# Performance work log

Hardware: AMD Instinct MI355X
Metric: run time of the kernel (lower is better)

The kernel has to match this reference:

```python
import jax, jax.numpy as jnp
import numpy as np

N = 50_000
E = 1_600_000
C_IN, C_HID, C_OUT, M = 128, 128, 2, 4


def gcn_norm(edge_index, num_nodes):
    # GCNConv default: add self-loops, symmetric normalization D^-1/2 (A+I) D^-1/2
    src, dst = edge_index[0], edge_index[1]
    loop = jnp.arange(num_nodes, dtype=edge_index.dtype)
    src = jnp.concatenate([src, loop])
    dst = jnp.concatenate([dst, loop])
    deg = jax.ops.segment_sum(jnp.ones_like(dst, dtype=jnp.float32), dst,
                              num_segments=num_nodes)
    dinv = jnp.where(deg > 0, jax.lax.rsqrt(deg), 0.0)
    norm = dinv[src] * dinv[dst]  # [E+N]
    return src, dst, norm


def propagate(h, src, dst, norm, num_nodes):
    # gather -> scale -> scatter-add (the memory-bound core)
    return jax.ops.segment_sum(h[src] * norm[:, None], dst, num_segments=num_nodes)


def setup_inputs() -> dict:
    key = jax.random.key(0)
    k0, k1, k2, k3 = jax.random.split(key, 4)
    x = jax.random.normal(k0, (N, C_IN), dtype=jnp.float32)
    edge_index = jax.random.randint(k1, (2, E), 0, N, dtype=jnp.int32)
    W1 = jax.random.normal(k2, (C_IN, C_HID), dtype=jnp.float32) * (1.0 / np.sqrt(C_IN))
    b1 = jnp.zeros((C_HID,), dtype=jnp.float32)
    W_out = jax.random.normal(k3, (M, C_HID, C_OUT), dtype=jnp.float32) * (1.0 / np.sqrt(C_HID))
    b_out = jnp.zeros((M, C_OUT), dtype=jnp.float32)
    return {"x": x, "edge_index": edge_index, "W1": W1, "b1": b1,
            "W_out": W_out, "b_out": b_out}


def reference(x, edge_index, W1, b1, W_out, b_out):
    n = x.shape[0]
    src, dst, norm = gcn_norm(edge_index, n)
    # hidden GCNConv + ReLU
    h = x @ W1                                  # [N, C_HID]
    h = propagate(h, src, dst, norm, n) + b1    # [N, C_HID]
    h = jax.nn.relu(h)
    # m output GCNConv heads. GCN propagation is linear in features, so
    # A_hat(h W_m) == (A_hat h) W_m: share one graph traversal across heads.
    agg = propagate(h, src, dst, norm, n)       # [N, C_HID]
    out = jnp.einsum('nf,mfo->mno', agg, W_out) + b_out[:, None, :]  # [M, N, C_OUT]
    return out
```

## Files before the change

kernel.cpp:

```cpp
#include <hip/hip_runtime.h>


constexpr int CIN = 128;
constexpr int SSHIFT = 8;
constexpr int NBLKB = 256;
constexpr int CSR_CAP = 10240;

typedef __attribute__((ext_vector_type(8))) short short8v;
typedef __attribute__((ext_vector_type(4))) float float4v;

__device__ inline unsigned pack_bf16x2(float a, float b) {
  unsigned ua = __float_as_uint(a), ub = __float_as_uint(b);
  ua = (ua + 0x7FFFu + ((ua >> 16) & 1u)) >> 16;
  ub = (ub + 0x7FFFu + ((ub >> 16) & 1u)) >> 16;
  return ua | (ub << 16);
}
__device__ inline float bf_lo(unsigned u) { return __uint_as_float(u << 16); }
__device__ inline float bf_hi(unsigned u) { return __uint_as_float(u & 0xFFFF0000u); }
__device__ inline unsigned short round_bf16(float v) {
  unsigned ua = __float_as_uint(v);
  return (unsigned short)((ua + 0x7FFFu + ((ua >> 16) & 1u)) >> 16);
}
__device__ inline void split1(float v, unsigned short& h, unsigned short& lo) {
  unsigned ua = __float_as_uint(v);
  unsigned hb = (ua + 0x7FFFu + ((ua >> 16) & 1u)) >> 16;
  float fh = __uint_as_float(hb << 16);
  float rl = v - fh;
  unsigned ub = __float_as_uint(rl);
  h = (unsigned short)hb;
  lo = (unsigned short)((ub + 0x7FFFu + ((ub >> 16) & 1u)) >> 16);
}

__global__ __launch_bounds__(256) void histsb_k(const int* __restrict__ dst,
    int* __restrict__ blockhist, int E, int nsb) {
  __shared__ int lh[256];
  int b = blockIdx.x, t = threadIdx.x;
  lh[t] = 0;
  __syncthreads();
  int per = (E + gridDim.x - 1) / gridDim.x;
  int s0 = b * per, s1 = min(E, s0 + per);
  for (int i = s0 + t; i < s1; i += 256) atomicAdd(&lh[dst[i] >> SSHIFT], 1);
  __syncthreads();
  if (t < nsb) blockhist[t * NBLKB + b] = lh[t];
}

__global__ __launch_bounds__(256) void scan_k(const int* __restrict__ v_in,
    int* __restrict__ excl_out, int* __restrict__ btot, int n) {
  __shared__ int wsum[4];
  int t = threadIdx.x, l = t & 63, w = t >> 6;
  int i = blockIdx.x * 256 + t;
  int v = (i < n) ? v_in[i] : 0;
  int orig = v;
  #pragma unroll
  for (int off = 1; off < 64; off <<= 1) {
    int u = __shfl_up(v, off);
    if (l >= off) v += u;
  }
  if (l == 63) wsum[w] = v;
  __syncthreads();
  int add = 0;
  #pragma unroll
  for (int j = 0; j < 4; ++j) if (j < w) add += wsum[j];
  v += add;
  if (i < n) excl_out[i] = v - orig;
  if (t == 255) btot[blockIdx.x] = v;
}

__global__ __launch_bounds__(256) void stageB_k(const int* __restrict__ src,
    const int* __restrict__ dst, const int* __restrict__ soff,
    const int* __restrict__ btot, unsigned* __restrict__ stage, int E, int nsb) {
  __shared__ int loff[256];
  __shared__ int wsum[4];
  int b = blockIdx.x, t = threadIdx.x, l = t & 63, w = t >> 6;
  int bv = (t < nsb) ? btot[t] : 0;
  int vv = bv;
  #pragma unroll
  for (int o = 1; o < 64; o <<= 1) { int u = __shfl_up(vv, o); if (l >= o) vv += u; }
  if (l == 63) wsum[w] = vv;
  __syncthreads();
  int add = 0;
  #pragma unroll
  for (int j = 0; j < 4; ++j) if (j < w) add += wsum[j];
  int bexcl = vv + add - bv;
  if (t < nsb) loff[t] = soff[t * NBLKB + b] + bexcl;
  __syncthreads();
  int per = (E + gridDim.x - 1) / gridDim.x;
  int s0 = b * per, s1 = min(E, s0 + per);
  for (int i = s0 + t; i < s1; i += 256) {
    int d = dst[i], s = src[i];
    int pos = atomicAdd(&loff[d >> SSHIFT], 1);
    stage[pos] = (unsigned)s | ((unsigned)(d & 255) << 17);
  }
}

__global__ __launch_bounds__(256) void csrsb_k(const unsigned* __restrict__ stage,
    const int* __restrict__ btot, int* __restrict__ row_ptr, int* __restrict__ csr,
    float* __restrict__ dinv, int N, int E, int nsb) {
  __shared__ int cnt[256], off[256], cur[256], sboff[256];
  __shared__ unsigned ebuf[CSR_CAP];
  __shared__ int sbuf[CSR_CAP];
  __shared__ int wsum[4];
  int k = blockIdx.x, t = threadIdx.x, l = t & 63, w = t >> 6;
  cnt[t] = 0; cur[t] = 0;
  {
    int bv = (t < nsb) ? btot[t] : 0;
    int vv = bv;
    #pragma unroll
    for (int o = 1; o < 64; o <<= 1) { int u = __shfl_up(vv, o); if (l >= o) vv += u; }
    if (l == 63) wsum[w] = vv;
    __syncthreads();
    int add = 0;
    #pragma unroll
    for (int j = 0; j < 4; ++j) if (j < w) add += wsum[j];
    sboff[t] = vv + add - bv;
  }
  __syncthreads();
  int r0 = sboff[k];
  int r1 = (k + 1 < nsb) ? sboff[k + 1] : E;
  int len = r1 - r0;
  bool fits = len <= CSR_CAP;
  if (fits) {
    for (int i = t; i < len; i += 256) {
      unsigned s = stage[r0 + i];
      ebuf[i] = s;
      atomicAdd(&cnt[s >> 17], 1);
    }
  } else {
    for (int i = r0 + t; i < r1; i += 256) atomicAdd(&cnt[stage[i] >> 17], 1);
  }
  __syncthreads();
  {
    int v = cnt[t], orig = v;
    #pragma unroll
    for (int o = 1; o < 64; o <<= 1) {
      int u = __shfl_up(v, o);
      if (l >= o) v += u;
    }
    if (l == 63) wsum[w] = v;
    __syncthreads();
    int add = 0;
    #pragma unroll
    for (int j = 0; j < 4; ++j) if (j < w) add += wsum[j];
    int excl = v + add - orig;
    off[t] = excl;
    int n = (k << SSHIFT) + t;
    if (n < N) {
      row_ptr[n] = r0 + excl;
      dinv[n] = rsqrtf((float)(orig + 1));
    }
    if (k == nsb - 1 && t == 255) row_ptr[N] = E;
  }
  __syncthreads();
  if (fits) {
    for (int i = t; i < len; i += 256) {
      unsigned s = ebuf[i];
      int dl = s >> 17;
      int pos = off[dl] + atomicAdd(&cur[dl], 1);
      sbuf[pos] = (int)(s & 0x1FFFF);
    }
    __syncthreads();
    for (int i = t; i < len; i += 256) csr[r0 + i] = sbuf[i];
  } else {
    for (int i = r0 + t; i < r1; i += 256) {
      unsigned s = stage[i];
      int dl = s >> 17;
      int pos = r0 + off[dl] + atomicAdd(&cur[dl], 1);
      csr[pos] = (int)(s & 0x1FFFF);
    }
  }
}

__global__ __launch_bounds__(256) void gemm_k(const float* __restrict__ x,
    const float* __restrict__ W, const float* __restrict__ dinv,
    unsigned* __restrict__ gu, int nrows) {
  __shared__ unsigned short Bh[16384];
  __shared__ unsigned short Bl[16384];
  __shared__ unsigned short Ah[4096];
  int t = threadIdx.x, l = t & 63, w = t >> 6;
  for (int idx = t; idx < 16384; idx += 256) {
    int k = idx >> 7, col = idx & 127;
    unsigned short hb, lb;
    split1(W[idx], hb, lb);
    int addr = (((k >> 5) * 8 + (col >> 4)) * 64 +
                (((k >> 3) & 3) * 16 + (col & 15))) * 8 + (k & 7);
    Bh[addr] = hb;
    Bl[addr] = lb;
  }

  int row0 = blockIdx.x * 128;
  int ct0 = w * 2;
  float4v acc[8][2];
  #pragma unroll
  for (int i = 0; i < 8; ++i) { acc[i][0] = (float4v)0.f; acc[i][1] = (float4v)0.f; }
  int arow = l & 15;
  int kg = l >> 4;
  int srow = t >> 1, skh = t & 1;
  int sgrow = min(row0 + srow, nrows - 1);

  for (int ks = 0; ks < 4; ++ks) {
    __syncthreads();
    {
      const float* xp = &x[(size_t)sgrow * CIN + ks * 32 + skh * 16];
      float f[16];
      *(float4*)&f[0]  = *(const float4*)xp;
      *(float4*)&f[4]  = *(const float4*)(xp + 4);
      *(float4*)&f[8]  = *(const float4*)(xp + 8);
      *(float4*)&f[12] = *(const float4*)(xp + 12);
      #pragma unroll
      for (int h = 0; h < 2; ++h) {
        short8v ah_;
        #pragma unroll
        for (int j = 0; j < 8; ++j) ah_[j] = (short)round_bf16(f[h * 8 + j]);
        int g = skh * 2 + h;
        *(short8v*)&Ah[(g * 128 + srow) * 8] = ah_;
      }
    }
    __syncthreads();
    short8v bh0 = *(short8v*)&Bh[((ks * 8 + ct0) * 64 + l) * 8];
    short8v bh1 = *(short8v*)&Bh[((ks * 8 + ct0 + 1) * 64 + l) * 8];
    short8v bl0 = *(short8v*)&Bl[((ks * 8 + ct0) * 64 + l) * 8];
    short8v bl1 = *(short8v*)&Bl[((ks * 8 + ct0 + 1) * 64 + l) * 8];
    #pragma unroll
    for (int rt = 0; rt < 8; ++rt) {
      int ar = arow + rt * 16;
      short8v ah = *(short8v*)&Ah[(kg * 128 + ar) * 8];
      acc[rt][0] = __builtin_amdgcn_mfma_f32_16x16x32_bf16(ah, bh0, acc[rt][0], 0, 0, 0);
      acc[rt][1] = __builtin_amdgcn_mfma_f32_16x16x32_bf16(ah, bh1, acc[rt][1], 0, 0, 0);
      acc[rt][0] = __builtin_amdgcn_mfma_f32_16x16x32_bf16(ah, bl0, acc[rt][0], 0, 0, 0);
      acc[rt][1] = __builtin_amdgcn_mfma_f32_16x16x32_bf16(ah, bl1, acc[rt][1], 0, 0, 0);
    }
  }
  #pragma unroll
  for (int rt = 0; rt < 8; ++rt) {
    #pragma unroll
    for (int r = 0; r < 4; ++r) {
      int row = row0 + rt * 16 + (l >> 4) * 4 + r;
      bool ok = row < nrows;
      float dv = ok ? dinv[row] : 0.f;
      #pragma unroll
      for (int c = 0; c < 2; ++c) {
        float val = acc[rt][c][r] * dv;
        float other = __shfl_xor(val, 1);
        int col = (ct0 + c) * 16 + (l & 15);
        if (ok && !(l & 1)) gu[(size_t)row * 64 + (col >> 1)] = pack_bf16x2(val, other);
      }
    }
  }
}

#define ACC8(U) do { \
  acc[0] += bf_lo((U).x); acc[1] += bf_hi((U).x); \
  acc[2] += bf_lo((U).y); acc[3] += bf_hi((U).y); \
  acc[4] += bf_lo((U).z); acc[5] += bf_hi((U).z); \
  acc[6] += bf_lo((U).w); acc[7] += bf_hi((U).w); } while (0)

__global__ __launch_bounds__(256) void prop1_k(const uint4* __restrict__ g4,
    const int* __restrict__ row_ptr, const int* __restrict__ csr,
    const float* __restrict__ dinv, const float* __restrict__ b1,
    const float* __restrict__ Wout, unsigned* __restrict__ g2w,
    int n_nodes, int n_waves) {
  int l = threadIdx.x & 63;
  int q = l & 15, sub = l >> 4;
  int wid = (blockIdx.x * blockDim.x + threadIdx.x) >> 6;
  float wj0[8], wj1[8], bb[8];
  #pragma unroll
  for (int c = 0; c < 8; ++c) {
    int col = 8 * q + c;
    wj0[c] = Wout[sub * 256 + col * 2];
    wj1[c] = Wout[sub * 256 + col * 2 + 1];
    bb[c] = b1[col];
  }
  for (int n = wid; n < n_nodes; n += n_waves) {
    int start = row_ptr[n], end = row_ptr[n + 1];
    float d = dinv[n];
    float acc[8];
    #pragma unroll
    for (int c = 0; c < 8; ++c) acc[c] = 0.f;
    for (int base = start; base < end; base += 64) {
      int cnt = min(64, end - base);
      int eb = (base + l < end) ? csr[base + l] : 0;
      int i = 0;
      for (; i + 16 <= cnt; i += 16) {
        int s0 = __shfl(eb, i + sub);
        int s1 = __shfl(eb, i + 4 + sub);
        int s2 = __shfl(eb, i + 8 + sub);
        int s3 = __shfl(eb, i + 12 + sub);
        uint4 u0 = g4[s0 * 16 + q];
        uint4 u1 = g4[s1 * 16 + q];
        uint4 u2 = g4[s2 * 16 + q];
        uint4 u3 = g4[s3 * 16 + q];
        ACC8(u0); ACC8(u1); ACC8(u2); ACC8(u3);
      }
      for (; i + 4 <= cnt; i += 4) {
        int s0 = __shfl(eb, i + sub);
        uint4 u0 = g4[s0 * 16 + q];
        ACC8(u0);
      }
      if (i < cnt) {
        int idx = i + sub;
        bool vld = idx < cnt;
        int s0 = __shfl(eb, vld ? idx : i);
        uint4 u0 = g4[s0 * 16 + q];
        if (vld) { ACC8(u0); }
      }
    }
    #pragma unroll
    for (int c = 0; c < 8; ++c) {
      acc[c] += __shfl_xor(acc[c], 16);
      acc[c] += __shfl_xor(acc[c], 32);
    }
    uint4 us = g4[n * 16 + q];
    ACC8(us);
    float p0 = 0.f, p1 = 0.f;
    #pragma unroll
    for (int c = 0; c < 8; ++c) {
      float y = fmaxf(fmaf(acc[c], d, bb[c]), 0.f);
      p0 = fmaf(y, wj0[c], p0);
      p1 = fmaf(y, wj1[c], p1);
    }
    #pragma unroll
    for (int off = 1; off < 16; off <<= 1) {
      p0 += __shfl_xor(p0, off);
      p1 += __shfl_xor(p1, off);
    }
    if (q == 0) g2w[n * 4 + sub] = pack_bf16x2(d * p0, d * p1);
  }
}

__global__ __launch_bounds__(256) void prop2_k(const uint2* __restrict__ g2v,
    const int* __restrict__ row_ptr, const int* __restrict__ csr,
    const float* __restrict__ dinv, const float* __restrict__ bout,
    float* __restrict__ out, int N) {
  int tid = blockIdx.x * 256 + threadIdx.x;
  int n = tid >> 1, hf = tid & 1;
  if (n >= N) return;
  uint2 us = g2v[n * 2 + hf];
  float a0 = bf_lo(us.x), a1 = bf_hi(us.x);
  float a2 = bf_lo(us.y), a3 = bf_hi(us.y);
  int e = row_ptr[n], e1 = row_ptr[n + 1];
  for (; e + 8 <= e1; e += 8) {
    int i0 = csr[e],     i1 = csr[e + 1], i2 = csr[e + 2], i3 = csr[e + 3];
    int i4 = csr[e + 4], i5 = csr[e + 5], i6 = csr[e + 6], i7 = csr[e + 7];
    uint2 u0 = g2v[i0 * 2 + hf], u1 = g2v[i1 * 2 + hf];
    uint2 u2 = g2v[i2 * 2 + hf], u3 = g2v[i3 * 2 + hf];
    uint2 u4 = g2v[i4 * 2 + hf], u5 = g2v[i5 * 2 + hf];
    uint2 u6 = g2v[i6 * 2 + hf], u7 = g2v[i7 * 2 + hf];
    a0 += ((bf_lo(u0.x) + bf_lo(u1.x)) + (bf_lo(u2.x) + bf_lo(u3.x)))
        + ((bf_lo(u4.x) + bf_lo(u5.x)) + (bf_lo(u6.x) + bf_lo(u7.x)));
    a1 += ((bf_hi(u0.x) + bf_hi(u1.x)) + (bf_hi(u2.x) + bf_hi(u3.x)))
        + ((bf_hi(u4.x) + bf_hi(u5.x)) + (bf_hi(u6.x) + bf_hi(u7.x)));
    a2 += ((bf_lo(u0.y) + bf_lo(u1.y)) + (bf_lo(u2.y) + bf_lo(u3.y)))
        + ((bf_lo(u4.y) + bf_lo(u5.y)) + (bf_lo(u6.y) + bf_lo(u7.y)));
    a3 += ((bf_hi(u0.y) + bf_hi(u1.y)) + (bf_hi(u2.y) + bf_hi(u3.y)))
        + ((bf_hi(u4.y) + bf_hi(u5.y)) + (bf_hi(u6.y) + bf_hi(u7.y)));
  }
  for (; e + 4 <= e1; e += 4) {
    int i0 = csr[e], i1 = csr[e + 1], i2 = csr[e + 2], i3 = csr[e + 3];
    uint2 u0 = g2v[i0 * 2 + hf], u1 = g2v[i1 * 2 + hf];
    uint2 u2 = g2v[i2 * 2 + hf], u3 = g2v[i3 * 2 + hf];
    a0 += (bf_lo(u0.x) + bf_lo(u1.x)) + (bf_lo(u2.x) + bf_lo(u3.x));
    a1 += (bf_hi(u0.x) + bf_hi(u1.x)) + (bf_hi(u2.x) + bf_hi(u3.x));
    a2 += (bf_lo(u0.y) + bf_lo(u1.y)) + (bf_lo(u2.y) + bf_lo(u3.y));
    a3 += (bf_hi(u0.y) + bf_hi(u1.y)) + (bf_hi(u2.y) + bf_hi(u3.y));
  }
  for (; e < e1; ++e) {
    uint2 u = g2v[csr[e] * 2 + hf];
    a0 += bf_lo(u.x); a1 += bf_hi(u.x);
    a2 += bf_lo(u.y); a3 += bf_hi(u.y);
  }
  float d = dinv[n];
  float2 o0 = make_float2(fmaf(d, a0, bout[hf * 4 + 0]), fmaf(d, a1, bout[hf * 4 + 1]));
  float2 o1 = make_float2(fmaf(d, a2, bout[hf * 4 + 2]), fmaf(d, a3, bout[hf * 4 + 3]));
  *(float2*)&out[(size_t)(hf * 2 + 0) * (2 * N) + 2 * n] = o0;
  *(float2*)&out[(size_t)(hf * 2 + 1) * (2 * N) + 2 * n] = o1;
}

extern "C" void kernel_launch(void* const* d_in, const int* in_sizes, int n_in,
                              void* d_out, int out_size, void* d_ws, size_t ws_size,
                              hipStream_t stream) {
  const float* x    = (const float*)d_in[0];
  const int*   ei   = (const int*)d_in[1];
  const float* W1   = (const float*)d_in[2];
  const float* b1   = (const float*)d_in[3];
  const float* Wout = (const float*)d_in[4];
  const float* bout = (const float*)d_in[5];
  float* out = (float*)d_out;

  const int N = in_sizes[0] / CIN;
  const int E = in_sizes[1] / 2;
  const int* srcp = ei;
  const int* dstp = ei + E;
  const int NSB = (N + 255) >> SSHIFT;
  const int NSC = NSB * NBLKB;

  char* ws = (char*)d_ws;
  size_t off = 0;
  auto alloc = [&](size_t bytes) -> void* {
    void* p = ws + off;
    off = (off + bytes + 511) & ~(size_t)511;
    return p;
  };
  unsigned*       gu        = (unsigned*)alloc((size_t)N * 64 * 4);
  unsigned short* g2u       = (unsigned short*)alloc((size_t)N * 8 * 2);
  float*          dinv      = (float*)alloc((size_t)N * 4);
  int*            blockhist = (int*)alloc((size_t)NSC * 4);
  int*            soff      = (int*)alloc((size_t)NSC * 4);
  int*            btot      = (int*)alloc(256 * 4);
  int*            row_ptr   = (int*)alloc((size_t)(N + 1) * 4);
  int*            csr       = (int*)alloc((size_t)E * 4);
  unsigned*       stage     = (unsigned*)alloc((size_t)E * 4);
  (void)ws_size; (void)n_in; (void)out_size;

  histsb_k<<<NBLKB, 256, 0, stream>>>(dstp, blockhist, E, NSB);
  scan_k<<<NSB, 256, 0, stream>>>(blockhist, soff, btot, NSC);
  stageB_k<<<NBLKB, 256, 0, stream>>>(srcp, dstp, soff, btot, stage, E, NSB);
  csrsb_k<<<NSB, 256, 0, stream>>>(stage, btot, row_ptr, csr, dinv, N, E, NSB);

  gemm_k<<<(N + 127) / 128, 256, 0, stream>>>(x, W1, dinv, gu, N);

  const int P1_BLOCKS = 2048;
  prop1_k<<<P1_BLOCKS, 256, 0, stream>>>((const uint4*)gu, row_ptr, csr, dinv, b1,
                                         Wout, (unsigned*)g2u, N, P1_BLOCKS * 4);
  prop2_k<<<(2 * N + 255) / 256, 256, 0, stream>>>((const uint2*)g2u, row_ptr, csr,
                                                   dinv, bout, out, N);
}
```

Measured before the change: 133.1 us.

## Drop split-bf16 W1 GEMM, vectorize edge binning, split prop2 edges across threads

The hidden GEMM no longer uses the hi/lo bf16 split of W1. It runs a single bf16 MFMA pass, which halves MFMA work and B shared memory at the cost of accuracy in the first-layer product. The histogram and staging kernels now read dst/src as int4 with a per-block chunk rounded up to a multiple of 4, plus a scalar tail. prop2 assigns two threads per node half, each summing half the edge list, and combines them with a shuffle to raise parallelism.

```diff
diff --git a/kernel.cpp b/kernel.cpp
--- a/kernel.cpp
+++ b/kernel.cpp
@@ -21,15 +21,6 @@
   unsigned ua = __float_as_uint(v);
   return (unsigned short)((ua + 0x7FFFu + ((ua >> 16) & 1u)) >> 16);
 }
-__device__ inline void split1(float v, unsigned short& h, unsigned short& lo) {
-  unsigned ua = __float_as_uint(v);
-  unsigned hb = (ua + 0x7FFFu + ((ua >> 16) & 1u)) >> 16;
-  float fh = __uint_as_float(hb << 16);
-  float rl = v - fh;
-  unsigned ub = __float_as_uint(rl);
-  h = (unsigned short)hb;
-  lo = (unsigned short)((ub + 0x7FFFu + ((ub >> 16) & 1u)) >> 16);
-}
 
 __global__ __launch_bounds__(256) void histsb_k(const int* __restrict__ dst,
     int* __restrict__ blockhist, int E, int nsb) {
@@ -37,9 +28,17 @@
   int b = blockIdx.x, t = threadIdx.x;
   lh[t] = 0;
   __syncthreads();
-  int per = (E + gridDim.x - 1) / gridDim.x;
+  int per = (((E + NBLKB - 1) / NBLKB) + 3) & ~3;
   int s0 = b * per, s1 = min(E, s0 + per);
-  for (int i = s0 + t; i < s1; i += 256) atomicAdd(&lh[dst[i] >> SSHIFT], 1);
+  for (int i = s0 + 4 * t; i + 3 < s1; i += 1024) {
+    int4 d4 = *(const int4*)&dst[i];
+    atomicAdd(&lh[d4.x >> SSHIFT], 1);
+    atomicAdd(&lh[d4.y >> SSHIFT], 1);
+    atomicAdd(&lh[d4.z >> SSHIFT], 1);
+    atomicAdd(&lh[d4.w >> SSHIFT], 1);
+  }
+  int tail0 = s0 + ((s1 - s0) & ~3);
+  for (int i = tail0 + t; i < s1; i += 256) atomicAdd(&lh[dst[i] >> SSHIFT], 1);
   __syncthreads();
   if (t < nsb) blockhist[t * NBLKB + b] = lh[t];
 }
@@ -84,9 +83,22 @@
   int bexcl = vv + add - bv;
   if (t < nsb) loff[t] = soff[t * NBLKB + b] + bexcl;
   __syncthreads();
-  int per = (E + gridDim.x - 1) / gridDim.x;
+  int per = (((E + NBLKB - 1) / NBLKB) + 3) & ~3;
   int s0 = b * per, s1 = min(E, s0 + per);
-  for (int i = s0 + t; i < s1; i += 256) {
+  for (int i = s0 + 4 * t; i + 3 < s1; i += 1024) {
+    int4 d4 = *(const int4*)&dst[i];
+    int4 s4 = *(const int4*)&src[i];
+    int p0 = atomicAdd(&loff[d4.x >> SSHIFT], 1);
+    stage[p0] = (unsigned)s4.x | ((unsigned)(d4.x & 255) << 17);
+    int p1 = atomicAdd(&loff[d4.y >> SSHIFT], 1);
+    stage[p1] = (unsigned)s4.y | ((unsigned)(d4.y & 255) << 17);
+    int p2 = atomicAdd(&loff[d4.z >> SSHIFT], 1);
+    stage[p2] = (unsigned)s4.z | ((unsigned)(d4.z & 255) << 17);
+    int p3 = atomicAdd(&loff[d4.w >> SSHIFT], 1);
+    stage[p3] = (unsigned)s4.w | ((unsigned)(d4.w & 255) << 17);
+  }
+  int tail0 = s0 + ((s1 - s0) & ~3);
+  for (int i = tail0 + t; i < s1; i += 256) {
     int d = dst[i], s = src[i];
     int pos = atomicAdd(&loff[d >> SSHIFT], 1);
     stage[pos] = (unsigned)s | ((unsigned)(d & 255) << 17);
@@ -174,17 +186,13 @@
     const float* __restrict__ W, const float* __restrict__ dinv,
     unsigned* __restrict__ gu, int nrows) {
   __shared__ unsigned short Bh[16384];
-  __shared__ unsigned short Bl[16384];
   __shared__ unsigned short Ah[4096];
   int t = threadIdx.x, l = t & 63, w = t >> 6;
   for (int idx = t; idx < 16384; idx += 256) {
     int k = idx >> 7, col = idx & 127;
-    unsigned short hb, lb;
-    split1(W[idx], hb, lb);
     int addr = (((k >> 5) * 8 + (col >> 4)) * 64 +
                 (((k >> 3) & 3) * 16 + (col & 15))) * 8 + (k & 7);
-    Bh[addr] = hb;
-    Bl[addr] = lb;
+    Bh[addr] = round_bf16(W[idx]);
   }
 
   int row0 = blockIdx.x * 128;
@@ -218,16 +226,12 @@
     __syncthreads();
     short8v bh0 = *(short8v*)&Bh[((ks * 8 + ct0) * 64 + l) * 8];
     short8v bh1 = *(short8v*)&Bh[((ks * 8 + ct0 + 1) * 64 + l) * 8];
-    short8v bl0 = *(short8v*)&Bl[((ks * 8 + ct0) * 64 + l) * 8];
-    short8v bl1 = *(short8v*)&Bl[((ks * 8 + ct0 + 1) * 64 + l) * 8];
     #pragma unroll
     for (int rt = 0; rt < 8; ++rt) {
       int ar = arow + rt * 16;
       short8v ah = *(short8v*)&Ah[(kg * 128 + ar) * 8];
       acc[rt][0] = __builtin_amdgcn_mfma_f32_16x16x32_bf16(ah, bh0, acc[rt][0], 0, 0, 0);
       acc[rt][1] = __builtin_amdgcn_mfma_f32_16x16x32_bf16(ah, bh1, acc[rt][1], 0, 0, 0);
-      acc[rt][0] = __builtin_amdgcn_mfma_f32_16x16x32_bf16(ah, bl0, acc[rt][0], 0, 0, 0);
-      acc[rt][1] = __builtin_amdgcn_mfma_f32_16x16x32_bf16(ah, bl1, acc[rt][1], 0, 0, 0);
     }
   }
   #pragma unroll
@@ -332,12 +336,19 @@
     const float* __restrict__ dinv, const float* __restrict__ bout,
     float* __restrict__ out, int N) {
   int tid = blockIdx.x * 256 + threadIdx.x;
-  int n = tid >> 1, hf = tid & 1;
+  int n = tid >> 2;
   if (n >= N) return;
-  uint2 us = g2v[n * 2 + hf];
-  float a0 = bf_lo(us.x), a1 = bf_hi(us.x);
-  float a2 = bf_lo(us.y), a3 = bf_hi(us.y);
-  int e = row_ptr[n], e1 = row_ptr[n + 1];
+  int hf = tid & 1, part = (tid >> 1) & 1;
+  int start = row_ptr[n], end = row_ptr[n + 1];
+  int mid = start + ((end - start) >> 1);
+  int e  = part ? mid : start;
+  int e1 = part ? end : mid;
+  float a0 = 0.f, a1 = 0.f, a2 = 0.f, a3 = 0.f;
+  if (!part) {
+    uint2 us = g2v[n * 2 + hf];
+    a0 = bf_lo(us.x); a1 = bf_hi(us.x);
+    a2 = bf_lo(us.y); a3 = bf_hi(us.y);
+  }
   for (; e + 8 <= e1; e += 8) {
     int i0 = csr[e],     i1 = csr[e + 1], i2 = csr[e + 2], i3 = csr[e + 3];
     int i4 = csr[e + 4], i5 = csr[e + 5], i6 = csr[e + 6], i7 = csr[e + 7];
@@ -368,11 +379,17 @@
     a0 += bf_lo(u.x); a1 += bf_hi(u.x);
     a2 += bf_lo(u.y); a3 += bf_hi(u.y);
   }
-  float d = dinv[n];
-  float2 o0 = make_float2(fmaf(d, a0, bout[hf * 4 + 0]), fmaf(d, a1, bout[hf * 4 + 1]));
-  float2 o1 = make_float2(fmaf(d, a2, bout[hf * 4 + 2]), fmaf(d, a3, bout[hf * 4 + 3]));
-  *(float2*)&out[(size_t)(hf * 2 + 0) * (2 * N) + 2 * n] = o0;
-  *(float2*)&out[(size_t)(hf * 2 + 1) * (2 * N) + 2 * n] = o1;
+  a0 += __shfl_xor(a0, 2);
+  a1 += __shfl_xor(a1, 2);
+  a2 += __shfl_xor(a2, 2);
+  a3 += __shfl_xor(a3, 2);
+  if (!part) {
+    float d = dinv[n];
+    float2 o0 = make_float2(fmaf(d, a0, bout[hf * 4 + 0]), fmaf(d, a1, bout[hf * 4 + 1]));
+    float2 o1 = make_float2(fmaf(d, a2, bout[hf * 4 + 2]), fmaf(d, a3, bout[hf * 4 + 3]));
+    *(float2*)&out[(size_t)(hf * 2 + 0) * (2 * N) + 2 * n] = o0;
+    *(float2*)&out[(size_t)(hf * 2 + 1) * (2 * N) + 2 * n] = o1;
+  }
 }
 
 extern "C" void kernel_launch(void* const* d_in, const int* in_sizes, int n_in,
@@ -421,6 +438,6 @@
   const int P1_BLOCKS = 2048;
   prop1_k<<<P1_BLOCKS, 256, 0, stream>>>((const uint4*)gu, row_ptr, csr, dinv, b1,
                                          Wout, (unsigned*)g2u, N, P1_BLOCKS * 4);
-  prop2_k<<<(2 * N + 255) / 256, 256, 0, stream>>>((const uint2*)g2u, row_ptr, csr,
+  prop2_k<<<(4 * N + 255) / 256, 256, 0, stream>>>((const uint2*)g2u, row_ptr, csr,
                                                    dinv, bout, out, N);
 }
```

Measured after the change: 126.6 us. 1.05x faster.
